# Optimization experiments

Hardware: AMD Instinct MI355X
Metric: run time of the kernel (lower is better)

Reference implementation:

```python
import jax, jax.numpy as jnp
import numpy as np

B, T, C, H = 2, 2048, 1024, 16  # batch, seq, d_model, heads
D = C // H                       # head dim = 64


def setup_inputs() -> dict:
    key = jax.random.key(0)
    ks = jax.random.split(key, 5)
    s = 0.02  # init scale for weights
    return {
        "x": jax.random.normal(ks[0], (B, T, C), jnp.float32),
        "Wq": jax.random.normal(ks[1], (C, C), jnp.float32) * s,
        "bq": jnp.zeros((C,), jnp.float32),
        "Wk": jax.random.normal(ks[2], (C, C), jnp.float32) * s,
        "bk": jnp.zeros((C,), jnp.float32),
        "Wv": jax.random.normal(ks[3], (C, C), jnp.float32) * s,
        "bv": jnp.zeros((C,), jnp.float32),
        "Wo": jax.random.normal(ks[4], (C, C), jnp.float32) * s,
        "bo": jnp.zeros((C,), jnp.float32),
    }


def reference(x, Wq, bq, Wk, bk, Wv, bv, Wo, bo):
    b, t, c = x.shape
    h, d = H, C // H
    # QKV projections (torch Linear: x @ W.T + b), split into heads: b h t d
    q = (x @ Wq.T + bq).reshape(b, t, h, d).transpose(0, 2, 1, 3)
    k = (x @ Wk.T + bk).reshape(b, t, h, d).transpose(0, 2, 1, 3)
    v = (x @ Wv.T + bv).reshape(b, t, h, d).transpose(0, 2, 1, 3)

    scale = 1.0 / float(np.sqrt(d))
    att = jnp.einsum("bhqd,bhkd->bhqk", q, k) * scale  # [B,H,T,T]
    causal = jnp.tril(jnp.ones((t, t), dtype=bool))
    att = jnp.where(causal[None, None, :, :], att, -jnp.inf)
    att = jax.nn.softmax(att, axis=-1)
    att_weights = att  # attn_dropout with p=0 is identity

    y = jnp.einsum("bhqk,bhkd->bhqd", att, v)          # [B,H,T,D]
    y = y.transpose(0, 2, 1, 3).reshape(b, t, c)        # b q (h d)
    y = y @ Wo.T + bo                                   # out proj; resid_dropout p=0
    return y, att_weights
```

## Files before the change

### kernel.cpp

```cpp
#include <hip/hip_runtime.h>

#define DI __device__ __forceinline__

typedef __attribute__((ext_vector_type(8))) short short8;
typedef __attribute__((ext_vector_type(4))) float floatx4;
typedef unsigned short u16;

#define Bb 2
#define Tt 2048
#define Cc 1024
#define Hh 16
#define Dd 64
#define C1 0.1803368801111244f
#define NEGBIG (-1e30f)

DI float bf2f(u16 u) { union { unsigned int i; float f; } v; v.i = ((unsigned int)u) << 16; return v.f; }
DI u16 f2bf(float f) {
  union { float f; unsigned int i; } v; v.f = f;
  unsigned int i = v.i;
  unsigned int r = i + 0x7fffu + ((i >> 16) & 1u);
  return (u16)(r >> 16);
}

DI floatx4 mfma16(short8 a, short8 b, floatx4 c) {
  return __builtin_amdgcn_mfma_f32_16x16x32_bf16(a, b, c, 0, 0, 0);
}

DI uint4 load8(const void* p, size_t eoff, int isbf) {
  if (isbf) {
    return *(const uint4*)((const u16*)p + eoff);
  } else {
    const float* f = (const float*)p + eoff;
    float4 a = *(const float4*)f;
    float4 b = *(const float4*)(f + 4);
    union { uint4 u; u16 s[8]; } r;
    r.s[0] = f2bf(a.x); r.s[1] = f2bf(a.y); r.s[2] = f2bf(a.z); r.s[3] = f2bf(a.w);
    r.s[4] = f2bf(b.x); r.s[5] = f2bf(b.y); r.s[6] = f2bf(b.z); r.s[7] = f2bf(b.w);
    return r.u;
  }
}

DI float loadb(const void* p, int i, int isbf) {
  return isbf ? bf2f(((const u16*)p)[i]) : ((const float*)p)[i];
}

__global__ void detect_dtype(const u16* __restrict__ x, int* __restrict__ flag) {
  __shared__ int cnt[256];
  int c = 0;
  for (int i = threadIdx.x; i < 4096; i += 256) {
    unsigned u = x[2 * i];
    unsigned e = (u >> 7) & 0xFFu;
    c += (e == 0u || (e >= 100u && e <= 150u)) ? 1 : 0;
  }
  cnt[threadIdx.x] = c;
  __syncthreads();
  for (int s = 128; s > 0; s >>= 1) {
    if ((int)threadIdx.x < s) cnt[threadIdx.x] += cnt[threadIdx.x + s];
    __syncthreads();
  }
  if (threadIdx.x == 0) *flag = (cnt[0] > 2458) ? 1 : 0;
}

__global__ __launch_bounds__(256) void qkv_gemm(
    const void* __restrict__ X,
    const void* __restrict__ Wq, const void* __restrict__ Wk, const void* __restrict__ Wv,
    const void* __restrict__ bq, const void* __restrict__ bk, const void* __restrict__ bv,
    u16* __restrict__ Qb, u16* __restrict__ Kb, u16* __restrict__ Vb,
    const int* __restrict__ flagp) {
  __shared__ __align__(16) u16 As[128 * 40];
  __shared__ __align__(16) u16 Bs[128 * 40];
  const int isbf = *flagp;
  const int z = blockIdx.z;
  const void* W = (z == 0) ? Wq : (z == 1) ? Wk : Wv;
  const void* bias = (z == 0) ? bq : (z == 1) ? bk : bv;
  u16* Out = (z == 0) ? Qb : (z == 1) ? Kb : Vb;

  const int m0 = blockIdx.y * 128, n0 = blockIdx.x * 128;
  const int tid = threadIdx.x;
  const int w = tid >> 6, lane = tid & 63, quad = lane >> 4, l15 = lane & 15;
  const int wm = w >> 1, wn = w & 1;

  floatx4 acc[4][4];
#pragma unroll
  for (int a = 0; a < 4; ++a)
#pragma unroll
    for (int b2 = 0; b2 < 4; ++b2) acc[a][b2] = (floatx4){0.f, 0.f, 0.f, 0.f};

  for (int k0 = 0; k0 < Cc; k0 += 32) {
    __syncthreads();
#pragma unroll
    for (int i = 0; i < 2; ++i) {
      int slot = tid + i * 256;
      int row = slot >> 2, c8 = slot & 3;
      *(uint4*)(As + row * 40 + c8 * 8) = load8(X, (size_t)(m0 + row) * Cc + k0 + c8 * 8, isbf);
      *(uint4*)(Bs + row * 40 + c8 * 8) = load8(W, (size_t)(n0 + row) * Cc + k0 + c8 * 8, isbf);
    }
    __syncthreads();
    short8 af[4], bfv[4];
#pragma unroll
    for (int t = 0; t < 4; ++t)
      af[t] = *(const short8*)(As + (wm * 64 + t * 16 + l15) * 40 + quad * 8);
#pragma unroll
    for (int t = 0; t < 4; ++t)
      bfv[t] = *(const short8*)(Bs + (wn * 64 + t * 16 + l15) * 40 + quad * 8);
#pragma unroll
    for (int tm = 0; tm < 4; ++tm)
#pragma unroll
      for (int tn = 0; tn < 4; ++tn) acc[tm][tn] = mfma16(af[tm], bfv[tn], acc[tm][tn]);
  }

  float bb[4];
#pragma unroll
  for (int tn = 0; tn < 4; ++tn) bb[tn] = loadb(bias, n0 + wn * 64 + tn * 16 + l15, isbf);
#pragma unroll
  for (int tm = 0; tm < 4; ++tm) {
#pragma unroll
    for (int tn = 0; tn < 4; ++tn) {
      int n = n0 + wn * 64 + tn * 16 + l15;
      int h = n >> 6, d = n & 63;
#pragma unroll
      for (int r = 0; r < 4; ++r) {
        int m = m0 + wm * 64 + tm * 16 + quad * 4 + r;
        int b = m >> 11, t = m & 2047;
        Out[(((size_t)(b * Hh + h) * Tt) + t) * Dd + d] = f2bf(acc[tm][tn][r] + bb[tn]);
      }
    }
  }
}

__global__ __launch_bounds__(256) void out_gemm(
    const u16* __restrict__ Y, const void* __restrict__ Wo, const void* __restrict__ bo,
    float* __restrict__ Out, const int* __restrict__ flagp) {
  __shared__ __align__(16) u16 As[128 * 40];
  __shared__ __align__(16) u16 Bs[128 * 40];
  const int isbf = *flagp;
  const int m0 = blockIdx.y * 128, n0 = blockIdx.x * 128;
  const int tid = threadIdx.x;
  const int w = tid >> 6, lane = tid & 63, quad = lane >> 4, l15 = lane & 15;
  const int wm = w >> 1, wn = w & 1;

  floatx4 acc[4][4];
#pragma unroll
  for (int a = 0; a < 4; ++a)
#pragma unroll
    for (int b2 = 0; b2 < 4; ++b2) acc[a][b2] = (floatx4){0.f, 0.f, 0.f, 0.f};

  for (int k0 = 0; k0 < Cc; k0 += 32) {
    __syncthreads();
#pragma unroll
    for (int i = 0; i < 2; ++i) {
      int slot = tid + i * 256;
      int row = slot >> 2, c8 = slot & 3;
      *(uint4*)(As + row * 40 + c8 * 8) = *(const uint4*)(Y + (size_t)(m0 + row) * Cc + k0 + c8 * 8);
      *(uint4*)(Bs + row * 40 + c8 * 8) = load8(Wo, (size_t)(n0 + row) * Cc + k0 + c8 * 8, isbf);
    }
    __syncthreads();
    short8 af[4], bfv[4];
#pragma unroll
    for (int t = 0; t < 4; ++t)
      af[t] = *(const short8*)(As + (wm * 64 + t * 16 + l15) * 40 + quad * 8);
#pragma unroll
    for (int t = 0; t < 4; ++t)
      bfv[t] = *(const short8*)(Bs + (wn * 64 + t * 16 + l15) * 40 + quad * 8);
#pragma unroll
    for (int tm = 0; tm < 4; ++tm)
#pragma unroll
      for (int tn = 0; tn < 4; ++tn) acc[tm][tn] = mfma16(af[tm], bfv[tn], acc[tm][tn]);
  }

  float bb[4];
#pragma unroll
  for (int tn = 0; tn < 4; ++tn) bb[tn] = loadb(bo, n0 + wn * 64 + tn * 16 + l15, isbf);
#pragma unroll
  for (int tm = 0; tm < 4; ++tm)
#pragma unroll
    for (int tn = 0; tn < 4; ++tn) {
      int n = n0 + wn * 64 + tn * 16 + l15;
#pragma unroll
      for (int r = 0; r < 4; ++r) {
        int m = m0 + wm * 64 + tm * 16 + quad * 4 + r;
        Out[(size_t)m * Cc + n] = acc[tm][tn][r] + bb[tn];
      }
    }
}

__global__ __launch_bounds__(256) void attn_kernel(
    const u16* __restrict__ Qbuf, const u16* __restrict__ Kbuf, const u16* __restrict__ Vbuf,
    float* __restrict__ Att, u16* __restrict__ Ybuf) {
  __shared__ __align__(16) u16 Qs[16 * 72];
  __shared__ __align__(16) u16 Ks[128 * 72];
  __shared__ __align__(16) u16 Vts[64 * 136];
  __shared__ __align__(16) u16 Ps[16 * 136];
  __shared__ float redM[4][16], redL[4][16];
  __shared__ float Mfin[16], Lfin[16];

  const int qt = blockIdx.x, h = blockIdx.y, b = blockIdx.z;
  const int q0 = qt * 16, q_hi = q0 + 15;
  const int tid = threadIdx.x;
  const int w = tid >> 6, lane = tid & 63, quad = lane >> 4, l15 = lane & 15;

  const size_t headoff = (size_t)(b * Hh + h) * Tt * Dd;
  const u16* Qh = Qbuf + headoff;
  const u16* Kh = Kbuf + headoff;
  const u16* Vh = Vbuf + headoff;
  float* attO = Att + (size_t)(b * Hh + h) * Tt * Tt;

  {
    int row = tid >> 4, c4 = tid & 15;
    *(uint2*)(Qs + row * 72 + c4 * 4) = *(const uint2*)(Qh + (size_t)(q0 + row) * Dd + c4 * 4);
  }
  __syncthreads();
  short8 aq0 = *(const short8*)(Qs + l15 * 72 + quad * 8);
  short8 aq1 = *(const short8*)(Qs + l15 * 72 + 32 + quad * 8);

  float m4[4], l4[4];
#pragma unroll
  for (int r = 0; r < 4; ++r) { m4[r] = NEGBIG; l4[r] = 0.f; }

  const int nact = (q_hi + 1 + 127) / 128;

  for (int c = 0; c < nact; ++c) {
    const int kb = c * 128;
    __syncthreads();
#pragma unroll
    for (int i = 0; i < 4; ++i) {
      int slot = tid + i * 256;
      int row = slot >> 3, c8 = slot & 7;
      *(uint4*)(Ks + row * 72 + c8 * 8) = *(const uint4*)(Kh + (size_t)(kb + row) * Dd + c8 * 8);
    }
    __syncthreads();
#pragma unroll
    for (int tile = 0; tile < 2; ++tile) {
      int kloc = w * 32 + tile * 16;
      floatx4 acc = (floatx4){0.f, 0.f, 0.f, 0.f};
      short8 b0 = *(const short8*)(Ks + (kloc + l15) * 72 + quad * 8);
      short8 b1 = *(const short8*)(Ks + (kloc + l15) * 72 + 32 + quad * 8);
      acc = mfma16(aq0, b0, acc);
      acc = mfma16(aq1, b1, acc);
      int key = kb + kloc + l15;
#pragma unroll
      for (int r = 0; r < 4; ++r) {
        int qi = q0 + quad * 4 + r;
        if (key <= qi) {
          float s2 = acc[r] * C1;
          float mo = m4[r];
          float mn = fmaxf(mo, s2);
          l4[r] = l4[r] * exp2f(mo - mn) + exp2f(s2 - mn);
          m4[r] = mn;
        }
      }
    }
  }

#pragma unroll
  for (int r = 0; r < 4; ++r) {
    float m = m4[r], l = l4[r];
#pragma unroll
    for (int off = 8; off >= 1; off >>= 1) {
      float mo = __shfl_xor(m, off, 64);
      float lo = __shfl_xor(l, off, 64);
      float mn = fmaxf(m, mo);
      l = l * exp2f(m - mn) + lo * exp2f(mo - mn);
      m = mn;
    }
    m4[r] = m; l4[r] = l;
  }
  if (l15 == 0) {
#pragma unroll
    for (int r = 0; r < 4; ++r) { redM[w][quad * 4 + r] = m4[r]; redL[w][quad * 4 + r] = l4[r]; }
  }
  __syncthreads();
  if (tid < 16) {
    float m = NEGBIG;
#pragma unroll
    for (int w2 = 0; w2 < 4; ++w2) m = fmaxf(m, redM[w2][tid]);
    float l = 0.f;
#pragma unroll
    for (int w2 = 0; w2 < 4; ++w2) l += redL[w2][tid] * exp2f(redM[w2][tid] - m);
    Mfin[tid] = m;
    Lfin[tid] = 1.0f / l;
  }
  __syncthreads();

  floatx4 yacc = (floatx4){0.f, 0.f, 0.f, 0.f};

  for (int c = 0; c < Tt / 128; ++c) {
    const int kb = c * 128;
    if (kb > q_hi) {
      uint4 z; z.x = 0u; z.y = 0u; z.z = 0u; z.w = 0u;
#pragma unroll
      for (int i = 0; i < 2; ++i) {
        int slot = tid + i * 256;
        int row = slot >> 5, g = slot & 31;
        *(uint4*)(attO + (size_t)(q0 + row) * Tt + kb + g * 4) = z;
      }
      continue;
    }
    __syncthreads();
#pragma unroll
    for (int i = 0; i < 4; ++i) {
      int slot = tid + i * 256;
      int row = slot >> 3, c8 = slot & 7;
      *(uint4*)(Ks + row * 72 + c8 * 8) = *(const uint4*)(Kh + (size_t)(kb + row) * Dd + c8 * 8);
    }
    {
      int row = tid >> 1, cb = (tid & 1) * 32;
      const u16* src = Vh + (size_t)(kb + row) * Dd + cb;
      union { uint4 u; u16 s[8]; } cv;
#pragma unroll
      for (int g = 0; g < 4; ++g) {
        cv.u = *(const uint4*)(src + g * 8);
#pragma unroll
        for (int j = 0; j < 8; ++j) Vts[(cb + g * 8 + j) * 136 + row] = cv.s[j];
      }
    }
    __syncthreads();

#pragma unroll
    for (int tile = 0; tile < 2; ++tile) {
      int kloc = w * 32 + tile * 16;
      floatx4 acc = (floatx4){0.f, 0.f, 0.f, 0.f};
      short8 b0 = *(const short8*)(Ks + (kloc + l15) * 72 + quad * 8);
      short8 b1 = *(const short8*)(Ks + (kloc + l15) * 72 + 32 + quad * 8);
      acc = mfma16(aq0, b0, acc);
      acc = mfma16(aq1, b1, acc);
      int key = kb + kloc + l15;
#pragma unroll
      for (int r = 0; r < 4; ++r) {
        int row = quad * 4 + r;
        int qi = q0 + row;
        float p = 0.f;
        if (key <= qi) p = exp2f(fminf(acc[r] * C1 - Mfin[row], 0.f)) * Lfin[row];
        attO[(size_t)qi * Tt + key] = p;
        Ps[row * 136 + kloc + l15] = f2bf(p);
      }
    }
    __syncthreads();

#pragma unroll
    for (int ks = 0; ks < 4; ++ks) {
      short8 ap = *(const short8*)(Ps + l15 * 136 + ks * 32 + quad * 8);
      short8 bv = *(const short8*)(Vts + (w * 16 + l15) * 136 + ks * 32 + quad * 8);
      yacc = mfma16(ap, bv, yacc);
    }
  }

#pragma unroll
  for (int r = 0; r < 4; ++r) {
    int qi = q0 + quad * 4 + r;
    Ybuf[(size_t)(b * Tt + qi) * Cc + h * Dd + w * 16 + l15] = f2bf(yacc[r]);
  }
}

extern "C" void kernel_launch(void* const* d_in, const int* in_sizes, int n_in,
                              void* d_out, int out_size, void* d_ws, size_t ws_size,
                              hipStream_t stream) {
  const void* x  = d_in[0];
  const void* Wq = d_in[1];
  const void* bq = d_in[2];
  const void* Wk = d_in[3];
  const void* bk = d_in[4];
  const void* Wv = d_in[5];
  const void* bv = d_in[6];
  const void* Wo = d_in[7];
  const void* bo = d_in[8];
  float* out = (float*)d_out;

  char* wsb = (char*)d_ws;
  int* flag = (int*)wsb;
  u16* Qb = (u16*)(wsb + 256);
  u16* Kb = Qb + (size_t)Bb * Tt * Cc;
  u16* Vb = Kb + (size_t)Bb * Tt * Cc;
  u16* Yb = Vb + (size_t)Bb * Tt * Cc;

  hipLaunchKernelGGL(detect_dtype, dim3(1), dim3(256), 0, stream, (const u16*)x, flag);
  hipLaunchKernelGGL(qkv_gemm, dim3(8, 32, 3), dim3(256), 0, stream,
                     x, Wq, Wk, Wv, bq, bk, bv, Qb, Kb, Vb, flag);
  float* attOut = out + (size_t)Bb * Tt * Cc;
  hipLaunchKernelGGL(attn_kernel, dim3(Tt / 16, Hh, Bb), dim3(256), 0, stream,
                     Qb, Kb, Vb, attOut, Yb);
  hipLaunchKernelGGL(out_gemm, dim3(8, 32, 1), dim3(256), 0, stream,
                     Yb, Wo, bo, out, flag);
}
```

Before: 870.8 us.

## Pre-convert inputs to bf16 and use direct global-to-LDS loads in GEMMs

Measured after the change: 796.3 us. 8.6% less time.

```diff
diff --git a/kernel.cpp b/kernel.cpp
--- a/kernel.cpp
+++ b/kernel.cpp
@@ -24,6 +24,12 @@
 
 DI floatx4 mfma16(short8 a, short8 b, floatx4 c) {
   return __builtin_amdgcn_mfma_f32_16x16x32_bf16(a, b, c, 0, 0, 0);
+}
+
+DI void gload16(const u16* g, u16* l) {
+  __builtin_amdgcn_global_load_lds(
+      (const __attribute__((address_space(1))) unsigned int*)(g),
+      (__attribute__((address_space(3))) unsigned int*)(l), 16, 0, 0);
 }
 
 DI uint4 load8(const void* p, size_t eoff, int isbf) {
@@ -61,17 +67,44 @@
   if (threadIdx.x == 0) *flag = (cnt[0] > 2458) ? 1 : 0;
 }
 
+__global__ __launch_bounds__(256) void convert_all(
+    const void* __restrict__ x,
+    const void* __restrict__ wq, const void* __restrict__ wk,
+    const void* __restrict__ wv, const void* __restrict__ wo,
+    u16* __restrict__ xb,
+    u16* __restrict__ wqb, u16* __restrict__ wkb,
+    u16* __restrict__ wvb, u16* __restrict__ wob,
+    const int* __restrict__ flagp) {
+  const int isbf = *flagp;
+  const void* src;
+  u16* dst;
+  size_t n;
+  switch (blockIdx.y) {
+    case 0: src = x;  dst = xb;  n = (size_t)Bb * Tt * Cc; break;
+    case 1: src = wq; dst = wqb; n = (size_t)Cc * Cc; break;
+    case 2: src = wk; dst = wkb; n = (size_t)Cc * Cc; break;
+    case 3: src = wv; dst = wvb; n = (size_t)Cc * Cc; break;
+    default: src = wo; dst = wob; n = (size_t)Cc * Cc; break;
+  }
+  size_t i8 = ((size_t)blockIdx.x * 256 + threadIdx.x) * 8;
+  size_t step = (size_t)gridDim.x * 256 * 8;
+  for (; i8 < n; i8 += step) {
+    uint4 v = load8(src, i8, isbf);
+    *(uint4*)(dst + i8) = v;
+  }
+}
+
 __global__ __launch_bounds__(256) void qkv_gemm(
-    const void* __restrict__ X,
-    const void* __restrict__ Wq, const void* __restrict__ Wk, const void* __restrict__ Wv,
+    const u16* __restrict__ Xb,
+    const u16* __restrict__ Wqb, const u16* __restrict__ Wkb, const u16* __restrict__ Wvb,
     const void* __restrict__ bq, const void* __restrict__ bk, const void* __restrict__ bv,
     u16* __restrict__ Qb, u16* __restrict__ Kb, u16* __restrict__ Vb,
     const int* __restrict__ flagp) {
-  __shared__ __align__(16) u16 As[128 * 40];
-  __shared__ __align__(16) u16 Bs[128 * 40];
+  __shared__ __align__(16) u16 As[128 * 32];
+  __shared__ __align__(16) u16 Bs[128 * 32];
   const int isbf = *flagp;
   const int z = blockIdx.z;
-  const void* W = (z == 0) ? Wq : (z == 1) ? Wk : Wv;
+  const u16* W = (z == 0) ? Wqb : (z == 1) ? Wkb : Wvb;
   const void* bias = (z == 0) ? bq : (z == 1) ? bk : bv;
   u16* Out = (z == 0) ? Qb : (z == 1) ? Kb : Vb;
 
@@ -86,23 +119,32 @@
 #pragma unroll
     for (int b2 = 0; b2 < 4; ++b2) acc[a][b2] = (floatx4){0.f, 0.f, 0.f, 0.f};
 
+  const int s0 = w * 128 + lane, s1 = s0 + 64;
+  const int rA0 = s0 >> 2, c0 = (s0 & 3) * 8;
+  const int rA1 = s1 >> 2, c1 = (s1 & 3) * 8;
+  const u16* gA0 = Xb + (size_t)(m0 + rA0) * Cc + c0;
+  const u16* gA1 = Xb + (size_t)(m0 + rA1) * Cc + c1;
+  const u16* gB0 = W + (size_t)(n0 + rA0) * Cc + c0;
+  const u16* gB1 = W + (size_t)(n0 + rA1) * Cc + c1;
+  u16* lA0 = As + w * 1024;
+  u16* lA1 = As + w * 1024 + 512;
+  u16* lB0 = Bs + w * 1024;
+  u16* lB1 = Bs + w * 1024 + 512;
+
   for (int k0 = 0; k0 < Cc; k0 += 32) {
     __syncthreads();
-#pragma unroll
-    for (int i = 0; i < 2; ++i) {
-      int slot = tid + i * 256;
-      int row = slot >> 2, c8 = slot & 3;
-      *(uint4*)(As + row * 40 + c8 * 8) = load8(X, (size_t)(m0 + row) * Cc + k0 + c8 * 8, isbf);
-      *(uint4*)(Bs + row * 40 + c8 * 8) = load8(W, (size_t)(n0 + row) * Cc + k0 + c8 * 8, isbf);
-    }
+    gload16(gA0 + k0, lA0);
+    gload16(gA1 + k0, lA1);
+    gload16(gB0 + k0, lB0);
+    gload16(gB1 + k0, lB1);
     __syncthreads();
     short8 af[4], bfv[4];
 #pragma unroll
     for (int t = 0; t < 4; ++t)
-      af[t] = *(const short8*)(As + (wm * 64 + t * 16 + l15) * 40 + quad * 8);
+      af[t] = *(const short8*)(As + (wm * 64 + t * 16 + l15) * 32 + quad * 8);
 #pragma unroll
     for (int t = 0; t < 4; ++t)
-      bfv[t] = *(const short8*)(Bs + (wn * 64 + t * 16 + l15) * 40 + quad * 8);
+      bfv[t] = *(const short8*)(Bs + (wn * 64 + t * 16 + l15) * 32 + quad * 8);
 #pragma unroll
     for (int tm = 0; tm < 4; ++tm)
 #pragma unroll
@@ -129,10 +171,10 @@
 }
 
 __global__ __launch_bounds__(256) void out_gemm(
-    const u16* __restrict__ Y, const void* __restrict__ Wo, const void* __restrict__ bo,
+    const u16* __restrict__ Y, const u16* __restrict__ Wob, const void* __restrict__ bo,
     float* __restrict__ Out, const int* __restrict__ flagp) {
-  __shared__ __align__(16) u16 As[128 * 40];
-  __shared__ __align__(16) u16 Bs[128 * 40];
+  __shared__ __align__(16) u16 As[128 * 32];
+  __shared__ __align__(16) u16 Bs[128 * 32];
   const int isbf = *flagp;
   const int m0 = blockIdx.y * 128, n0 = blockIdx.x * 128;
   const int tid = threadIdx.x;
@@ -145,23 +187,32 @@
 #pragma unroll
     for (int b2 = 0; b2 < 4; ++b2) acc[a][b2] = (floatx4){0.f, 0.f, 0.f, 0.f};
 
+  const int s0 = w * 128 + lane, s1 = s0 + 64;
+  const int rA0 = s0 >> 2, c0 = (s0 & 3) * 8;
+  const int rA1 = s1 >> 2, c1 = (s1 & 3) * 8;
+  const u16* gA0 = Y + (size_t)(m0 + rA0) * Cc + c0;
+  const u16* gA1 = Y + (size_t)(m0 + rA1) * Cc + c1;
+  const u16* gB0 = Wob + (size_t)(n0 + rA0) * Cc + c0;
+  const u16* gB1 = Wob + (size_t)(n0 + rA1) * Cc + c1;
+  u16* lA0 = As + w * 1024;
+  u16* lA1 = As + w * 1024 + 512;
+  u16* lB0 = Bs + w * 1024;
+  u16* lB1 = Bs + w * 1024 + 512;
+
   for (int k0 = 0; k0 < Cc; k0 += 32) {
     __syncthreads();
-#pragma unroll
-    for (int i = 0; i < 2; ++i) {
-      int slot = tid + i * 256;
-      int row = slot >> 2, c8 = slot & 3;
-      *(uint4*)(As + row * 40 + c8 * 8) = *(const uint4*)(Y + (size_t)(m0 + row) * Cc + k0 + c8 * 8);
-      *(uint4*)(Bs + row * 40 + c8 * 8) = load8(Wo, (size_t)(n0 + row) * Cc + k0 + c8 * 8, isbf);
-    }
+    gload16(gA0 + k0, lA0);
+    gload16(gA1 + k0, lA1);
+    gload16(gB0 + k0, lB0);
+    gload16(gB1 + k0, lB1);
     __syncthreads();
     short8 af[4], bfv[4];
 #pragma unroll
     for (int t = 0; t < 4; ++t)
-      af[t] = *(const short8*)(As + (wm * 64 + t * 16 + l15) * 40 + quad * 8);
+      af[t] = *(const short8*)(As + (wm * 64 + t * 16 + l15) * 32 + quad * 8);
 #pragma unroll
     for (int t = 0; t < 4; ++t)
-      bfv[t] = *(const short8*)(Bs + (wn * 64 + t * 16 + l15) * 40 + quad * 8);
+      bfv[t] = *(const short8*)(Bs + (wn * 64 + t * 16 + l15) * 32 + quad * 8);
 #pragma unroll
     for (int tm = 0; tm < 4; ++tm)
 #pragma unroll
@@ -366,19 +417,29 @@
   const void* bo = d_in[8];
   float* out = (float*)d_out;
 
+  const size_t NTC = (size_t)Bb * Tt * Cc;
+  const size_t CC = (size_t)Cc * Cc;
+
   char* wsb = (char*)d_ws;
   int* flag = (int*)wsb;
   u16* Qb = (u16*)(wsb + 256);
-  u16* Kb = Qb + (size_t)Bb * Tt * Cc;
-  u16* Vb = Kb + (size_t)Bb * Tt * Cc;
-  u16* Yb = Vb + (size_t)Bb * Tt * Cc;
+  u16* Kb = Qb + NTC;
+  u16* Vb = Kb + NTC;
+  u16* Yb = Vb + NTC;
+  u16* Xb = Yb + NTC;
+  u16* Wqb = Xb + NTC;
+  u16* Wkb = Wqb + CC;
+  u16* Wvb = Wkb + CC;
+  u16* Wob = Wvb + CC;
 
   hipLaunchKernelGGL(detect_dtype, dim3(1), dim3(256), 0, stream, (const u16*)x, flag);
+  hipLaunchKernelGGL(convert_all, dim3(512, 5), dim3(256), 0, stream,
+                     x, Wq, Wk, Wv, Wo, Xb, Wqb, Wkb, Wvb, Wob, flag);
   hipLaunchKernelGGL(qkv_gemm, dim3(8, 32, 3), dim3(256), 0, stream,
-                     x, Wq, Wk, Wv, bq, bk, bv, Qb, Kb, Vb, flag);
-  float* attOut = out + (size_t)Bb * Tt * Cc;
+                     Xb, Wqb, Wkb, Wvb, bq, bk, bv, Qb, Kb, Vb, flag);
+  float* attOut = out + NTC;
   hipLaunchKernelGGL(attn_kernel, dim3(Tt / 16, Hh, Bb), dim3(256), 0, stream,
                      Qb, Kb, Vb, attOut, Yb);
   hipLaunchKernelGGL(out_gemm, dim3(8, 32, 1), dim3(256), 0, stream,
-                     Yb, Wo, bo, out, flag);
-}
+                     Yb, Wob, bo, out, flag);
+}
```
